# Optimization experiments

Hardware: AMD Instinct MI355X
Metric: run time of the kernel (lower is better)

Reference implementation:

```python
import jax, jax.numpy as jnp
import numpy as np

B, L, D, OUT, EXP = 4, 4096, 128, 55, 2
D2 = 2 * D

def _ln(x, g, b):
    m = jnp.mean(x, axis=-1, keepdims=True)
    v = jnp.mean((x - m) ** 2, axis=-1, keepdims=True)
    return (x - m) / jnp.sqrt(v + 1e-5) * g + b

def setup_inputs() -> dict:
    key = jax.random.key(0)
    ks = iter(jax.random.split(key, 32))
    w = lambda shape: jax.random.normal(next(ks), shape, jnp.float32) * 0.02
    inp = {
        'x1': jax.random.normal(next(ks), (B, L, D), jnp.float32),
        'x2': jax.random.normal(next(ks), (B, L, D), jnp.float32),
        'ln1_g': jnp.ones((D,)), 'ln1_b': jnp.zeros((D,)),
        'ln2_g': jnp.ones((D,)), 'ln2_b': jnp.zeros((D,)),
        'Wq': w((D, D)), 'bq': jnp.zeros((D,)),
        'Wv1': w((D, D)), 'bv1': jnp.zeros((D,)),
        'Wk': w((D, D)), 'bk': jnp.zeros((D,)),
        'Wv2': w((D, D)), 'bv2': jnp.zeros((D,)),
        'Wp1': w((D, D)), 'bp1': jnp.zeros((D,)),
        'Wp2': w((D, D)), 'bp2': jnp.zeros((D,)),
        'lnf_g': jnp.ones((D2,)), 'lnf_b': jnp.zeros((D2,)),
        'Wf1': w((D2, EXP * D2)), 'bf1': jnp.zeros((EXP * D2,)),
        'Wf2': w((EXP * D2, D2)), 'bf2': jnp.zeros((D2,)),
        'ln3_g': jnp.ones((D2,)), 'ln3_b': jnp.zeros((D2,)),
        'Wo': w((D2, OUT)), 'bo': jnp.zeros((OUT,)),
    }
    return inp

def reference(x1, x2, ln1_g, ln1_b, ln2_g, ln2_b, Wq, bq, Wv1, bv1, Wk, bk,
              Wv2, bv2, Wp1, bp1, Wp2, bp2, lnf_g, lnf_b, Wf1, bf1, Wf2, bf2,
              ln3_g, ln3_b, Wo, bo):
    res1, res2 = x1, x2
    x1n = _ln(x1, ln1_g, ln1_b)
    x2n = _ln(x2, ln2_g, ln2_b)
    q1 = x1n @ Wq + bq        # [B,L,D]
    v1 = x1n @ Wv1 + bv1
    k2 = x2n @ Wk + bk
    v2 = x2n @ Wv2 + bv2
    # faithful to torch: energy = einsum('bqd,bkd->bqk', keys2, queries1)
    energy = jnp.einsum('bqd,bkd->bqk', k2, q1)
    att = jax.nn.softmax(energy / jnp.sqrt(jnp.float32(D)), axis=-1)  # [B,L,L]
    out1 = jnp.einsum('bal,blv->bav', att, v1) @ Wp1 + bp1
    out2 = jnp.einsum('bal,blv->bav', att, v2) @ Wp2 + bp2
    y1 = out1 + res1
    y2 = out2 + res2
    x = jnp.concatenate([y1, y2], axis=-1)  # [B,L,2D]
    res = x
    h = _ln(x, lnf_g, lnf_b)
    h = jax.nn.gelu(h @ Wf1 + bf1, approximate=False) @ Wf2 + bf2
    x = _ln(h + res, ln3_g, ln3_b)
    return x @ Wo + bo  # [B,L,OUT]
```

## Files before the change

### kernel.cpp

```cpp
#include <hip/hip_runtime.h>
#include <hip/hip_fp16.h>

typedef _Float16 half8 __attribute__((ext_vector_type(8)));
typedef _Float16 half4 __attribute__((ext_vector_type(4)));
typedef float f32x4 __attribute__((ext_vector_type(4)));
typedef float f32x16 __attribute__((ext_vector_type(16)));
typedef int  i32x8 __attribute__((ext_vector_type(8)));
typedef long lng2 __attribute__((ext_vector_type(2)));

#define B_   4
#define L_   4096
#define D_   128
#define M_   (B_*L_)
#define D2_  256
#define H_   512
#define OUT_ 55

__device__ __forceinline__ f32x4 mfma16(half8 a, half8 b, f32x4 c) {
    return __builtin_amdgcn_mfma_f32_16x16x32_f16(a, b, c, 0, 0, 0);
}
__device__ __forceinline__ f32x16 mfma_mx32(i32x8 a, i32x8 b, f32x16 c) {
    return __builtin_amdgcn_mfma_scale_f32_32x32x64_f8f6f4(a, b, c, 0, 0, 0, 127, 0, 127);
}
__device__ __forceinline__ int pk4(float a, float b, float c, float d) {
    int t = __builtin_amdgcn_cvt_pk_fp8_f32(a, b, 0, false);
    return __builtin_amdgcn_cvt_pk_fp8_f32(c, d, t, true);
}
__device__ __forceinline__ float fexp2(float x) { return __builtin_amdgcn_exp2f(x); }

#define KSCL (0.08838834764831845f * 1.4426950408889634f)

#define WQ_OFF   0
#define WV1_OFF  16384
#define WK_OFF   32768
#define WV2_OFF  49152
#define WP1_OFF  65536
#define WP2_OFF  81920
#define WF1_OFF  98304
#define WF2_OFF  229376
#define WO_OFF   360448


__global__ void prep_kernel(const float* Wq, const float* Wv1, const float* Wk,
                            const float* Wv2, const float* Wp1, const float* Wp2,
                            const float* Wf1, const float* Wf2, const float* Wo,
                            _Float16* wsw, float* rowsum) {
    int id = blockIdx.y;
    int t  = blockIdx.x * 256 + threadIdx.x;
    if (id == 9) {
        if (t < 4096) ((f32x4*)rowsum)[t] = f32x4{0.f, 0.f, 0.f, 0.f};
        return;
    }
    const float* src = nullptr; int K = 0, N = 0, Npad = 0, off = 0;
    switch (id) {
        case 0: src = Wq;  K = 128; N = 128; Npad = 128; off = WQ_OFF;  break;
        case 1: src = Wv1; K = 128; N = 128; Npad = 128; off = WV1_OFF; break;
        case 2: src = Wk;  K = 128; N = 128; Npad = 128; off = WK_OFF;  break;
        case 3: src = Wv2; K = 128; N = 128; Npad = 128; off = WV2_OFF; break;
        case 4: src = Wp1; K = 128; N = 128; Npad = 128; off = WP1_OFF; break;
        case 5: src = Wp2; K = 128; N = 128; Npad = 128; off = WP2_OFF; break;
        case 6: src = Wf1; K = 256; N = 512; Npad = 512; off = WF1_OFF; break;
        case 7: src = Wf2; K = 512; N = 256; Npad = 256; off = WF2_OFF; break;
        case 8: src = Wo;  K = 256; N = 55;  Npad = 64;  off = WO_OFF;  break;
        default: return;
    }
    int total = K * Npad;
    if (t >= total) return;
    int k = t / Npad, n = t % Npad;
    float v = (n < N) ? src[k * N + n] : 0.f;
    int s = k >> 5, c = n >> 4, ln = n & 15;
    int q, j;
    if (id == 4 || id == 5) { q = (k >> 2) & 3; j = (k & 3) + (((k >> 4) & 1) << 2); }
    else                    { q = (k >> 3) & 3; j = k & 7; }
    int nc = Npad >> 4;
    wsw[off + ((size_t)((s * nc + c) * 64 + q * 16 + ln)) * 8 + j] = (_Float16)v;
}


__global__ __launch_bounds__(256) void proj_kernel(const float* x1, const float* x2,
        const _Float16* wsw,
        const float* ln1_g, const float* ln1_b, const float* ln2_g, const float* ln2_b,
        const float* bq, const float* bv1, const float* bk, const float* bv2,
        _Float16* q1, _Float16* k2, unsigned char* vsw8) {
    int g2 = blockIdx.y;
    const float* X  = g2 ? x2 : x1;
    const float* lg = g2 ? ln2_g : ln1_g;
    const float* lb = g2 ? ln2_b : ln1_b;
    int wave = threadIdx.x >> 6, lane = threadIdx.x & 63;
    int quad = lane >> 4, ln = lane & 15;
    int mbase = blockIdx.x * 64 + wave * 16;
    int lt = mbase >> 4;

    const float* xr = X + (size_t)(mbase + ln) * D_;
    float xv[4][8];
    float sum = 0.f, sq = 0.f;
    #pragma unroll
    for (int s = 0; s < 4; s++) {
        f32x4 v0 = *(const f32x4*)(xr + s * 32 + quad * 8);
        f32x4 v1 = *(const f32x4*)(xr + s * 32 + quad * 8 + 4);
        #pragma unroll
        for (int j = 0; j < 4; j++) {
            xv[s][j]     = v0[j];
            xv[s][j + 4] = v1[j];
            sum += v0[j] + v1[j];
            sq  += v0[j] * v0[j] + v1[j] * v1[j];
        }
    }
    sum += __shfl_xor(sum, 16); sum += __shfl_xor(sum, 32);
    sq  += __shfl_xor(sq, 16);  sq  += __shfl_xor(sq, 32);
    float mean = sum * (1.f / 128.f);
    float var  = sq * (1.f / 128.f) - mean * mean;
    float inv  = rsqrtf(var + 1e-5f);
    half8 a[4];
    #pragma unroll
    for (int s = 0; s < 4; s++) {
        f32x4 g0 = *(const f32x4*)(lg + s * 32 + quad * 8);
        f32x4 g1 = *(const f32x4*)(lg + s * 32 + quad * 8 + 4);
        f32x4 b0 = *(const f32x4*)(lb + s * 32 + quad * 8);
        f32x4 b1 = *(const f32x4*)(lb + s * 32 + quad * 8 + 4);
        #pragma unroll
        for (int j = 0; j < 4; j++) {
            a[s][j]     = (_Float16)((xv[s][j] - mean) * inv * g0[j] + b0[j]);
            a[s][j + 4] = (_Float16)((xv[s][j + 4] - mean) * inv * g1[j] + b1[j]);
        }
    }

    {
        const _Float16* Bw = wsw + (g2 ? WK_OFF : WQ_OFF);
        const float* bias = g2 ? bk : bq;
        float scl = g2 ? KSCL : 1.f;
        _Float16* out = g2 ? k2 : q1;
        f32x4 acc[8];
        #pragma unroll
        for (int c = 0; c < 8; c++) acc[c] = f32x4{0.f, 0.f, 0.f, 0.f};
        half8 Wc[4], Wn[4];
        #pragma unroll
        for (int s = 0; s < 4; s++)
            Wc[s] = *(const half8*)(Bw + ((size_t)((s * 8 + 0) * 64 + lane)) * 8);
        #pragma unroll
        for (int c = 0; c < 8; c++) {
            int cn = (c < 7) ? c + 1 : 7;
            #pragma unroll
            for (int s = 0; s < 4; s++)
                Wn[s] = *(const half8*)(Bw + ((size_t)((s * 8 + cn) * 64 + lane)) * 8);
            #pragma unroll
            for (int s = 0; s < 4; s++)
                acc[c] = mfma16(a[s], Wc[s], acc[c]);
            #pragma unroll
            for (int s = 0; s < 4; s++) Wc[s] = Wn[s];
        }
        #pragma unroll
        for (int c = 0; c < 8; c++) {
            int n = c * 16 + ln;
            float bv = bias[n];
            #pragma unroll
            for (int r = 0; r < 4; r++) {
                int s_o = c >> 1, q_o = ((c & 1) << 1) | (ln >> 3), j = ln & 7;
                out[((size_t)((lt * 4 + s_o) * 64 + q_o * 16 + (quad * 4 + r))) * 8 + j]
                    = (_Float16)((acc[c][r] + bv) * scl);
            }
        }
    }

    {
        const _Float16* Bw = wsw + (g2 ? WV2_OFF : WV1_OFF);
        const float* bias = g2 ? bv2 : bv1;
        int cbase = g2 ? 8 : 0;
        f32x4 acc[8];
        #pragma unroll
        for (int c = 0; c < 8; c++) acc[c] = f32x4{0.f, 0.f, 0.f, 0.f};
        half8 Wc[4], Wn[4];
        #pragma unroll
        for (int s = 0; s < 4; s++)
            Wc[s] = *(const half8*)(Bw + ((size_t)((s * 8 + 0) * 64 + lane)) * 8);
        #pragma unroll
        for (int c = 0; c < 8; c++) {
            int cn = (c < 7) ? c + 1 : 7;
            #pragma unroll
            for (int s = 0; s < 4; s++)
                Wn[s] = *(const half8*)(Bw + ((size_t)((s * 8 + cn) * 64 + lane)) * 8);
            #pragma unroll
            for (int s = 0; s < 4; s++)
                acc[c] = mfma16(a[s], Wc[s], acc[c]);
            #pragma unroll
            for (int s = 0; s < 4; s++) Wc[s] = Wn[s];
        }
        int b = mbase >> 12;
        int k64 = (mbase & (L_ - 1)) >> 6;
        int gg = quad >> 1, jh = quad & 1;
        unsigned char* Vb = vsw8 + (size_t)b * (1u << 20);
        #pragma unroll
        for (int c = 0; c < 8; c++) {
            int n = c * 16 + ln;
            float bv = bias[n];
            int pk = pk4(acc[c][0] + bv, acc[c][1] + bv, acc[c][2] + bv, acc[c][3] + bv);
            int v32 = (cbase + c) >> 1;
            int lane32 = ((c & 1) << 4) + ln + 32 * gg;
            *(int*)(Vb + ((size_t)((k64 * 8 + v32) * 64 + lane32)) * 32 + 16 * jh + 4 * wave) = pk;
        }
    }
}

__global__ __launch_bounds__(256) void score_kernel(
        const _Float16* __restrict__ q1sw, const _Float16* __restrict__ k2sw,
        unsigned char* __restrict__ pmat8, float* __restrict__ rowsum) {
    int w = threadIdx.x >> 6, lane = threadIdx.x & 63;
    int quad = lane >> 4, ln = lane & 15;
    int b = blockIdx.z;
    int id0 = blockIdx.y * 32 + blockIdx.x;
    int id  = ((id0 & 7) << 7) + (id0 >> 3);
    int bx = id & 31, by = id >> 5;
    int kL0 = by * 128 + (w & 1) * 64;
    int mL0 = bx * 128 + (w >> 1) * 64;
    int ltk = ((b << 12) + kL0) >> 4;
    int ltm = ((b << 12) + mL0) >> 4;

    f32x4 acc[4][4];
    #pragma unroll
    for (int i = 0; i < 4; i++)
        #pragma unroll
        for (int j = 0; j < 4; j++) acc[i][j] = f32x4{0.f, 0.f, 0.f, 0.f};

    #pragma unroll
    for (int s = 0; s < 4; s++) {
        half8 a[4], bq[4];
        #pragma unroll
        for (int i = 0; i < 4; i++)
            a[i] = *(const half8*)(q1sw + ((size_t)(((ltk + i) * 4 + s) * 64 + lane)) * 8);
        #pragma unroll
        for (int j = 0; j < 4; j++)
            bq[j] = *(const half8*)(k2sw + ((size_t)(((ltm + j) * 4 + s) * 64 + lane)) * 8);
        #pragma unroll
        for (int i = 0; i < 4; i++)
            #pragma unroll
            for (int j = 0; j < 4; j++)
                acc[i][j] = mfma16(a[i], bq[j], acc[i][j]);
    }

    unsigned char* Pb = pmat8 + (size_t)b * (16u << 20);
    int k64 = kL0 >> 6;
    int gg = quad >> 1, jh = quad & 1;
    #pragma unroll
    for (int j = 0; j < 4; j++) {
        int4 d;
        float csum = 0.f;
        #pragma unroll
        for (int i = 0; i < 4; i++) {
            float p0 = fexp2(acc[i][j][0]);
            float p1 = fexp2(acc[i][j][1]);
            float p2 = fexp2(acc[i][j][2]);
            float p3 = fexp2(acc[i][j][3]);
            csum += (p0 + p1) + (p2 + p3);
            ((int*)&d)[i] = pk4(p0, p1, p2, p3);
        }
        csum += __shfl_xor(csum, 16);
        csum += __shfl_xor(csum, 32);
        if (lane < 16)
            atomicAdd(&rowsum[(b << 12) + mL0 + j * 16 + ln], csum);
        int att32 = (mL0 >> 5) + (j >> 1);
        int a32 = ((j & 1) << 4) + ln;
        *(int4*)(Pb + ((size_t)((att32 * 64 + k64) * 64 + a32 + 32 * gg)) * 32 + 16 * jh) = d;
    }
}

__global__ __launch_bounds__(512) void pv_kernel(
        const unsigned char* __restrict__ pmat8, const unsigned char* __restrict__ vsw8,
        const float* __restrict__ rowsum,
        _Float16* __restrict__ att1, _Float16* __restrict__ att2) {
    __shared__ f32x4 part[4][2][4][64];
    int w = threadIdx.x >> 6, lane = threadIdx.x & 63;
    int wc = w & 3, kh = w >> 2;
    int id0 = blockIdx.x;
    int bid = ((id0 & 7) << 6) + (id0 >> 3);
    int rowG0 = bid * 32;
    int b = rowG0 >> 12;
    int att32 = (rowG0 & (L_ - 1)) >> 5;
    const unsigned char* Pb = pmat8 + (size_t)b * (16u << 20);
    const unsigned char* Vb = vsw8 + (size_t)b * (1u << 20);

    const unsigned char* Vbase = Vb + (size_t)(wc * 2) * 2048 + (size_t)lane * 32;
    const unsigned char* Pbase = Pb + (size_t)att32 * 131072 + (size_t)lane * 32;
    int sp0 = kh * 32;

    f32x16 acc0, acc1;
    #pragma unroll
    for (int i = 0; i < 16; i++) { acc0[i] = 0.f; acc1[i] = 0.f; }

    #define PVLOAD(dA, dB, dP, sp) do {                                       \
        dA = *(const i32x8*)(Vbase + (size_t)(sp) * 16384);                   \
        dB = *(const i32x8*)(Vbase + (size_t)(sp) * 16384 + 2048);            \
        dP = *(const i32x8*)(Pbase + (size_t)(sp) * 2048);                    \
    } while (0)

    i32x8 a0, b0, p0, a1, b1, p1, na, nb, np;
    PVLOAD(a0, b0, p0, sp0);
    PVLOAD(a1, b1, p1, sp0 + 1);
    for (int ii = 0; ii < 32; ii += 2) {
        int s2 = sp0 + ((ii + 2 < 32) ? ii + 2 : 30);
        int s3 = sp0 + ((ii + 3 < 32) ? ii + 3 : 31);
        PVLOAD(na, nb, np, s2);
        __builtin_amdgcn_s_setprio(1);
        acc0 = mfma_mx32(a0, p0, acc0);
        acc1 = mfma_mx32(b0, p0, acc1);
        __builtin_amdgcn_s_setprio(0);
        a0 = na; b0 = nb; p0 = np;
        PVLOAD(na, nb, np, s3);
        __builtin_amdgcn_s_setprio(1);
        acc0 = mfma_mx32(a1, p1, acc0);
        acc1 = mfma_mx32(b1, p1, acc1);
        __builtin_amdgcn_s_setprio(0);
        a1 = na; b1 = nb; p1 = np;
    }
    #undef PVLOAD

    if (kh == 1) {
        #pragma unroll
        for (int q = 0; q < 4; q++) {
            part[wc][0][q][lane] = f32x4{acc0[q * 4 + 0], acc0[q * 4 + 1],
                                         acc0[q * 4 + 2], acc0[q * 4 + 3]};
            part[wc][1][q][lane] = f32x4{acc1[q * 4 + 0], acc1[q * 4 + 1],
                                         acc1[q * 4 + 2], acc1[q * 4 + 3]};
        }
    }
    __syncthreads();
    if (kh == 0) {
        int aglob = rowG0 + (lane & 31);
        float inv = 1.f / rowsum[aglob];
        int g = lane >> 5;
        int lt = aglob >> 4, lnr = lane & 15;
        #pragma unroll
        for (int t = 0; t < 2; t++) {
            int v32 = wc * 2 + t;
            _Float16* att = (v32 >= 4) ? att2 : att1;
            int s = v32 & 3;
            #pragma unroll
            for (int q = 0; q < 4; q++) {
                f32x4 pp = part[wc][t][q][lane];
                half4 hv;
                #pragma unroll
                for (int rr = 0; rr < 4; rr++) {
                    float v = ((t == 0) ? acc0[q * 4 + rr] : acc1[q * 4 + rr]) + pp[rr];
                    hv[rr] = (_Float16)(v * inv);
                }
                *(half4*)(att + ((size_t)((lt * 4 + s) * 64 + q * 16 + lnr)) * 8 + 4 * g) = hv;
            }
        }
    }
}

__global__ __launch_bounds__(256) void attn_out_kernel(const _Float16* att1, const _Float16* att2,
        const _Float16* wsw, const float* bp1, const float* bp2,
        const float* x1, const float* x2, const float* lnf_g, const float* lnf_b,
        _Float16* res, _Float16* xn) {
    __shared__ float sst[2][16][2][2];
    int w = threadIdx.x >> 6, lane = threadIdx.x & 63;
    int quad = lane >> 4, ln = lane & 15;
    int rt = w & 1, st = w >> 1;
    int mbase = blockIdx.x * 32 + rt * 16;
    int lt = mbase >> 4;
    const _Float16* att = st ? att2 : att1;
    const _Float16* Wp = wsw + (st ? WP2_OFF : WP1_OFF);
    const float* bp = st ? bp2 : bp1;
    const float* xres = st ? x2 : x1;

    half8 a[4];
    #pragma unroll
    for (int s = 0; s < 4; s++)
        a[s] = *(const half8*)(att + ((size_t)((lt * 4 + s) * 64 + lane)) * 8);

    f32x4 y[8];
    #pragma unroll
    for (int c = 0; c < 8; c++) y[c] = f32x4{0,0,0,0};

    half8 Wc[4], Wn[4];
    #pragma unroll
    for (int s = 0; s < 4; s++)
        Wc[s] = *(const half8*)(Wp + ((size_t)((s * 8 + 0) * 64 + lane)) * 8);
    #pragma unroll
    for (int c = 0; c < 8; c++) {
        int cn = (c < 7) ? c + 1 : 7;
        #pragma unroll
        for (int s = 0; s < 4; s++)
            Wn[s] = *(const half8*)(Wp + ((size_t)((s * 8 + cn) * 64 + lane)) * 8);
        #pragma unroll
        for (int s = 0; s < 4; s++)
            y[c] = mfma16(a[s], Wc[s], y[c]);
        #pragma unroll
        for (int s = 0; s < 4; s++) Wc[s] = Wn[s];
    }

    float psum[4] = {0,0,0,0}, psq[4] = {0,0,0,0};
    #pragma unroll
    for (int c = 0; c < 8; c++) {
        int n = c * 16 + ln;
        float bv = bp[n];
        #pragma unroll
        for (int r = 0; r < 4; r++) {
            int m = mbase + quad * 4 + r;
            float v = y[c][r] + bv + xres[(size_t)m * D_ + n];
            y[c][r] = v; psum[r] += v; psq[r] += v * v;
        }
    }
    #pragma unroll
    for (int off = 1; off < 16; off <<= 1)
        #pragma unroll
        for (int r = 0; r < 4; r++) { psum[r] += __shfl_xor(psum[r], off); psq[r] += __shfl_xor(psq[r], off); }
    if (ln == 0)
        #pragma unroll
        for (int r = 0; r < 4; r++) {
            sst[rt][quad * 4 + r][st][0] = psum[r];
            sst[rt][quad * 4 + r][st][1] = psq[r];
        }
    __syncthreads();
    #pragma unroll
    for (int r = 0; r < 4; r++) {
        float su = sst[rt][quad * 4 + r][0][0] + sst[rt][quad * 4 + r][1][0];
        float sq = sst[rt][quad * 4 + r][0][1] + sst[rt][quad * 4 + r][1][1];
        float mean = su * (1.f / 256.f);
        float var = sq * (1.f / 256.f) - mean * mean;
        float inv = rsqrtf(var + 1e-5f);
        int m = mbase + quad * 4 + r;
        int lt_m = m >> 4;
        #pragma unroll
        for (int c = 0; c < 8; c++) {
            int colg = st * 128 + c * 16 + ln;
            res[(size_t)m * D2_ + colg] = (_Float16)y[c][r];
            float yn = (y[c][r] - mean) * inv * lnf_g[colg] + lnf_b[colg];
            int s_x = colg >> 5, q_x = (colg >> 3) & 3, j = colg & 7;
            xn[((size_t)((lt_m * 8 + s_x) * 64 + q_x * 16 + (m & 15))) * 8 + j] = (_Float16)yn;
        }
    }
}

__global__ __launch_bounds__(512) void ffn_kernel(const _Float16* xn, const _Float16* wsw,
        const float* bf1, const float* bf2, const _Float16* res,
        const float* g3, const float* b3, const float* bo, float* out) {
    __shared__ _Float16 hT[16384];
    __shared__ float sst[2][16][4][2];
    __shared__ _Float16 xt[8192];
    __shared__ f32x4 pc[2][3][4][64];
    int w = threadIdx.x >> 6, lane = threadIdx.x & 63;
    int quad = lane >> 4, ln = lane & 15;
    int rt = w & 1, nh = w >> 1;
    int mb = blockIdx.x * 32;
    int ltg = (mb + rt * 16) >> 4;

    {
        const _Float16* W = wsw + WF1_OFF;
        half8 a[8];
        #pragma unroll
        for (int s = 0; s < 8; s++)
            a[s] = *(const half8*)(xn + ((size_t)((ltg * 8 + s) * 64 + lane)) * 8);
        f32x4 acc[8];
        #pragma unroll
        for (int c = 0; c < 8; c++) acc[c] = f32x4{0,0,0,0};
        #pragma unroll
        for (int c = 0; c < 8; c++) {
            #pragma unroll
            for (int s = 0; s < 8; s++) {
                half8 Wf = *(const half8*)(W + ((size_t)((s * 32 + nh * 8 + c) * 64 + lane)) * 8);
                acc[c] = mfma16(a[s], Wf, acc[c]);
            }
        }
        #pragma unroll
        for (int c = 0; c < 8; c++) {
            int n = nh * 128 + c * 16 + ln;
            float bv = bf1[n];
            int s_h = n >> 5, q_h = (n >> 3) & 3, j = n & 7;
            #pragma unroll
            for (int r = 0; r < 4; r++) {
                float v = acc[c][r] + bv;
                float u = 0.7978845608f * (v + 0.044715f * v * v * v);
                float e = fexp2(-2.8853900818f * u);
                float ge = v * __builtin_amdgcn_rcpf(1.f + e);
                hT[((rt * 16 + s_h) * 64 + q_h * 16 + (quad * 4 + r)) * 8 + j] = (_Float16)ge;
            }
        }
    }
    __syncthreads();

    float y[4][4];
    {
        const _Float16* W = wsw + WF2_OFF;
        f32x4 acc[4];
        #pragma unroll
        for (int c = 0; c < 4; c++) acc[c] = f32x4{0,0,0,0};
        #pragma unroll
        for (int s = 0; s < 16; s++) {
            half8 a = *(const half8*)(hT + ((size_t)((rt * 16 + s) * 64 + lane)) * 8);
            #pragma unroll
            for (int c = 0; c < 4; c++) {
                half8 Wf = *(const half8*)(W + ((size_t)((s * 16 + nh * 4 + c) * 64 + lane)) * 8);
                acc[c] = mfma16(a, Wf, acc[c]);
            }
        }
        float psum[4] = {0,0,0,0}, psq[4] = {0,0,0,0};
        #pragma unroll
        for (int c = 0; c < 4; c++) {
            int n = nh * 64 + c * 16 + ln;
            float bv = bf2[n];
            #pragma unroll
            for (int r = 0; r < 4; r++) {
                int m = mb + rt * 16 + quad * 4 + r;
                float v = acc[c][r] + bv + (float)res[(size_t)m * D2_ + n];
                y[c][r] = v; psum[r] += v; psq[r] += v * v;
            }
        }
        #pragma unroll
        for (int off = 1; off < 16; off <<= 1)
            #pragma unroll
            for (int r = 0; r < 4; r++) { psum[r] += __shfl_xor(psum[r], off); psq[r] += __shfl_xor(psq[r], off); }
        if (ln == 0)
            #pragma unroll
            for (int r = 0; r < 4; r++) { sst[rt][quad * 4 + r][nh][0] = psum[r]; sst[rt][quad * 4 + r][nh][1] = psq[r]; }
    }
    __syncthreads();
    #pragma unroll
    for (int r = 0; r < 4; r++) {
        int row = quad * 4 + r;
        float su = sst[rt][row][0][0] + sst[rt][row][1][0] + sst[rt][row][2][0] + sst[rt][row][3][0];
        float sq = sst[rt][row][0][1] + sst[rt][row][1][1] + sst[rt][row][2][1] + sst[rt][row][3][1];
        float mean = su * (1.f / 256.f);
        float var = sq * (1.f / 256.f) - mean * mean;
        float invs = rsqrtf(var + 1e-5f);
        #pragma unroll
        for (int c = 0; c < 4; c++) {
            int n = nh * 64 + c * 16 + ln;
            float yn = (y[c][r] - mean) * invs * g3[n] + b3[n];
            int s_x = n >> 5, q_x = (n >> 3) & 3, j = n & 7;
            xt[((rt * 8 + s_x) * 64 + q_x * 16 + row) * 8 + j] = (_Float16)yn;
        }
    }
    __syncthreads();

    {
        int kh = nh;
        const _Float16* Wo = wsw + WO_OFF;
        f32x4 oacc[4];
        #pragma unroll
        for (int c = 0; c < 4; c++) oacc[c] = f32x4{0,0,0,0};
        #pragma unroll
        for (int ss = 0; ss < 2; ss++) {
            int s = kh * 2 + ss;
            half8 a = *(const half8*)(xt + ((size_t)((rt * 8 + s) * 64 + lane)) * 8);
            #pragma unroll
            for (int c = 0; c < 4; c++)
                oacc[c] = mfma16(a, *(const half8*)(Wo + ((size_t)((s * 4 + c) * 64 + lane)) * 8), oacc[c]);
        }
        if (kh > 0)
            #pragma unroll
            for (int c = 0; c < 4; c++) pc[rt][kh - 1][c][lane] = oacc[c];
        __syncthreads();
        if (kh == 0) {
            #pragma unroll
            for (int c = 0; c < 4; c++) {
                f32x4 p0 = pc[rt][0][c][lane];
                f32x4 p1 = pc[rt][1][c][lane];
                f32x4 p2 = pc[rt][2][c][lane];
                int n = c * 16 + ln;
                if (n < OUT_) {
                    float bv = bo[n];
                    #pragma unroll
                    for (int r = 0; r < 4; r++)
                        out[(size_t)(mb + rt * 16 + quad * 4 + r) * OUT_ + n]
                            = oacc[c][r] + p0[r] + p1[r] + p2[r] + bv;
                }
            }
        }
    }
}

extern "C" void kernel_launch(void* const* d_in, const int* in_sizes, int n_in,
                              void* d_out, int out_size, void* d_ws, size_t ws_size,
                              hipStream_t stream) {
    const float* x1    = (const float*)d_in[0];
    const float* x2    = (const float*)d_in[1];
    const float* ln1_g = (const float*)d_in[2];
    const float* ln1_b = (const float*)d_in[3];
    const float* ln2_g = (const float*)d_in[4];
    const float* ln2_b = (const float*)d_in[5];
    const float* Wq    = (const float*)d_in[6];
    const float* bq    = (const float*)d_in[7];
    const float* Wv1   = (const float*)d_in[8];
    const float* bv1   = (const float*)d_in[9];
    const float* Wk    = (const float*)d_in[10];
    const float* bk    = (const float*)d_in[11];
    const float* Wv2   = (const float*)d_in[12];
    const float* bv2   = (const float*)d_in[13];
    const float* Wp1   = (const float*)d_in[14];
    const float* bp1   = (const float*)d_in[15];
    const float* Wp2   = (const float*)d_in[16];
    const float* bp2   = (const float*)d_in[17];
    const float* lnf_g = (const float*)d_in[18];
    const float* lnf_b = (const float*)d_in[19];
    const float* Wf1   = (const float*)d_in[20];
    const float* bf1   = (const float*)d_in[21];
    const float* Wf2   = (const float*)d_in[22];
    const float* bf2   = (const float*)d_in[23];
    const float* ln3_g = (const float*)d_in[24];
    const float* ln3_b = (const float*)d_in[25];
    const float* Wo    = (const float*)d_in[26];
    const float* bo    = (const float*)d_in[27];
    float* out = (float*)d_out;

    char* ws = (char*)d_ws;
    const size_t MB = 1 << 20;
    _Float16* q1sw   = (_Float16*)(ws + 0 * MB);
    _Float16* k2sw   = (_Float16*)(ws + 4 * MB);
    unsigned char* vsw8 = (unsigned char*)(ws + 8 * MB);
    _Float16* att1   = (_Float16*)(ws + 12 * MB);
    _Float16* att2   = (_Float16*)(ws + 16 * MB);
    _Float16* wsw    = (_Float16*)(ws + 28 * MB);
    float*    rowsum = (float*)   (ws + 29 * MB);
    _Float16* res    = (_Float16*)(ws + 30 * MB);
    _Float16* xn     = (_Float16*)(ws + 46 * MB);
    unsigned char* pmat8 = (unsigned char*)(ws + 78 * MB);

    prep_kernel<<<dim3(512, 10), 256, 0, stream>>>(Wq, Wv1, Wk, Wv2, Wp1, Wp2, Wf1, Wf2, Wo,
                                                   wsw, rowsum);
    proj_kernel<<<dim3(M_ / 64, 2), 256, 0, stream>>>(x1, x2, wsw,
                                                      ln1_g, ln1_b, ln2_g, ln2_b,
                                                      bq, bv1, bk, bv2,
                                                      q1sw, k2sw, vsw8);
    score_kernel<<<dim3(32, 32, 4), 256, 0, stream>>>(q1sw, k2sw, pmat8, rowsum);
    pv_kernel<<<dim3(M_ / 32), 512, 0, stream>>>(pmat8, vsw8, rowsum, att1, att2);
    attn_out_kernel<<<dim3(M_ / 32), 256, 0, stream>>>(att1, att2, wsw, bp1, bp2,
                                                       x1, x2, lnf_g, lnf_b, res, xn);
    ffn_kernel<<<dim3(M_ / 32), 512, 0, stream>>>(xn, wsw, bf1, bf2, res,
                                                  ln3_g, ln3_b, bo, out);
}
```

Before: 228.4 us.

## Fuse attention output projection and residual LayerNorm into PV kernel epilogue

The attn_out kernel is merged into the PV kernel. The normalized attention rows now stay in shared memory instead of making a round trip through global att1/att2 buffers. The output projection is split across all 8 waves along K, with partial sums reduced through the reused shared buffer, then bias, residual, LayerNorm, res and xn stores follow. This removes one kernel launch and the global write and read of the attention output, at the cost of extra shared memory, more barriers, and a longer tail in the PV kernel that may lower occupancy.

```diff
diff --git a/kernel.cpp b/kernel.cpp
--- a/kernel.cpp
+++ b/kernel.cpp
@@ -6,7 +6,6 @@
 typedef float f32x4 __attribute__((ext_vector_type(4)));
 typedef float f32x16 __attribute__((ext_vector_type(16)));
 typedef int  i32x8 __attribute__((ext_vector_type(8)));
-typedef long lng2 __attribute__((ext_vector_type(2)));
 
 #define B_   4
 #define L_   4096
@@ -265,10 +264,15 @@
 
 __global__ __launch_bounds__(512) void pv_kernel(
         const unsigned char* __restrict__ pmat8, const unsigned char* __restrict__ vsw8,
-        const float* __restrict__ rowsum,
-        _Float16* __restrict__ att1, _Float16* __restrict__ att2) {
+        const float* __restrict__ rowsum, const _Float16* __restrict__ wsw,
+        const float* bp1, const float* bp2,
+        const float* x1, const float* x2, const float* lnf_g, const float* lnf_b,
+        _Float16* __restrict__ res, _Float16* __restrict__ xn) {
     __shared__ f32x4 part[4][2][4][64];
+    __shared__ _Float16 attT[2][4096];
+    __shared__ float sstA[2][16][2][2];
     int w = threadIdx.x >> 6, lane = threadIdx.x & 63;
+    int quad = lane >> 4, ln = lane & 15;
     int wc = w & 3, kh = w >> 2;
     int id0 = blockIdx.x;
     int bid = ((id0 & 7) << 6) + (id0 >> 3);
@@ -324,14 +328,14 @@
     }
     __syncthreads();
     if (kh == 0) {
-        int aglob = rowG0 + (lane & 31);
-        float inv = 1.f / rowsum[aglob];
+        int rowL = lane & 31;
+        float inv = 1.f / rowsum[rowG0 + rowL];
         int g = lane >> 5;
-        int lt = aglob >> 4, lnr = lane & 15;
+        int ltl = rowL >> 4, lnr = lane & 15;
         #pragma unroll
         for (int t = 0; t < 2; t++) {
             int v32 = wc * 2 + t;
-            _Float16* att = (v32 >= 4) ? att2 : att1;
+            int stw = (v32 >= 4);
             int s = v32 & 3;
             #pragma unroll
             for (int q = 0; q < 4; q++) {
@@ -342,92 +346,90 @@
                     float v = ((t == 0) ? acc0[q * 4 + rr] : acc1[q * 4 + rr]) + pp[rr];
                     hv[rr] = (_Float16)(v * inv);
                 }
-                *(half4*)(att + ((size_t)((lt * 4 + s) * 64 + q * 16 + lnr)) * 8 + 4 * g) = hv;
-            }
-        }
-    }
-}
-
-__global__ __launch_bounds__(256) void attn_out_kernel(const _Float16* att1, const _Float16* att2,
-        const _Float16* wsw, const float* bp1, const float* bp2,
-        const float* x1, const float* x2, const float* lnf_g, const float* lnf_b,
-        _Float16* res, _Float16* xn) {
-    __shared__ float sst[2][16][2][2];
-    int w = threadIdx.x >> 6, lane = threadIdx.x & 63;
-    int quad = lane >> 4, ln = lane & 15;
-    int rt = w & 1, st = w >> 1;
-    int mbase = blockIdx.x * 32 + rt * 16;
-    int lt = mbase >> 4;
-    const _Float16* att = st ? att2 : att1;
-    const _Float16* Wp = wsw + (st ? WP2_OFF : WP1_OFF);
-    const float* bp = st ? bp2 : bp1;
-    const float* xres = st ? x2 : x1;
-
-    half8 a[4];
-    #pragma unroll
-    for (int s = 0; s < 4; s++)
-        a[s] = *(const half8*)(att + ((size_t)((lt * 4 + s) * 64 + lane)) * 8);
-
-    f32x4 y[8];
-    #pragma unroll
-    for (int c = 0; c < 8; c++) y[c] = f32x4{0,0,0,0};
-
-    half8 Wc[4], Wn[4];
-    #pragma unroll
-    for (int s = 0; s < 4; s++)
-        Wc[s] = *(const half8*)(Wp + ((size_t)((s * 8 + 0) * 64 + lane)) * 8);
-    #pragma unroll
-    for (int c = 0; c < 8; c++) {
-        int cn = (c < 7) ? c + 1 : 7;
-        #pragma unroll
-        for (int s = 0; s < 4; s++)
-            Wn[s] = *(const half8*)(Wp + ((size_t)((s * 8 + cn) * 64 + lane)) * 8);
-        #pragma unroll
-        for (int s = 0; s < 4; s++)
-            y[c] = mfma16(a[s], Wc[s], y[c]);
-        #pragma unroll
-        for (int s = 0; s < 4; s++) Wc[s] = Wn[s];
-    }
-
-    float psum[4] = {0,0,0,0}, psq[4] = {0,0,0,0};
-    #pragma unroll
-    for (int c = 0; c < 8; c++) {
-        int n = c * 16 + ln;
-        float bv = bp[n];
-        #pragma unroll
-        for (int r = 0; r < 4; r++) {
-            int m = mbase + quad * 4 + r;
-            float v = y[c][r] + bv + xres[(size_t)m * D_ + n];
-            y[c][r] = v; psum[r] += v; psq[r] += v * v;
-        }
-    }
-    #pragma unroll
-    for (int off = 1; off < 16; off <<= 1)
-        #pragma unroll
-        for (int r = 0; r < 4; r++) { psum[r] += __shfl_xor(psum[r], off); psq[r] += __shfl_xor(psq[r], off); }
-    if (ln == 0)
-        #pragma unroll
-        for (int r = 0; r < 4; r++) {
-            sst[rt][quad * 4 + r][st][0] = psum[r];
-            sst[rt][quad * 4 + r][st][1] = psq[r];
-        }
+                *(half4*)(&attT[stw][((ltl * 4 + s) * 64 + q * 16 + lnr) * 8 + 4 * g]) = hv;
+            }
+        }
+    }
     __syncthreads();
-    #pragma unroll
-    for (int r = 0; r < 4; r++) {
-        float su = sst[rt][quad * 4 + r][0][0] + sst[rt][quad * 4 + r][1][0];
-        float sq = sst[rt][quad * 4 + r][0][1] + sst[rt][quad * 4 + r][1][1];
-        float mean = su * (1.f / 256.f);
-        float var = sq * (1.f / 256.f) - mean * mean;
-        float inv = rsqrtf(var + 1e-5f);
-        int m = mbase + quad * 4 + r;
-        int lt_m = m >> 4;
+
+    {
+        int rt = w & 1, st = (w >> 1) & 1, kh2 = w >> 2;
+        const _Float16* Wp = wsw + (st ? WP2_OFF : WP1_OFF);
+        const float* bp = st ? bp2 : bp1;
+        const float* xres = st ? x2 : x1;
+
+        half8 a2[2];
+        #pragma unroll
+        for (int ss = 0; ss < 2; ss++)
+            a2[ss] = *(const half8*)(&attT[st][((rt * 4 + kh2 * 2 + ss) * 64 + lane) * 8]);
+
+        f32x4 y[8];
+        #pragma unroll
+        for (int c = 0; c < 8; c++) y[c] = f32x4{0,0,0,0};
         #pragma unroll
         for (int c = 0; c < 8; c++) {
-            int colg = st * 128 + c * 16 + ln;
-            res[(size_t)m * D2_ + colg] = (_Float16)y[c][r];
-            float yn = (y[c][r] - mean) * inv * lnf_g[colg] + lnf_b[colg];
-            int s_x = colg >> 5, q_x = (colg >> 3) & 3, j = colg & 7;
-            xn[((size_t)((lt_m * 8 + s_x) * 64 + q_x * 16 + (m & 15))) * 8 + j] = (_Float16)yn;
+            #pragma unroll
+            for (int ss = 0; ss < 2; ss++) {
+                half8 Wf = *(const half8*)(Wp + ((size_t)(((kh2 * 2 + ss) * 8 + c) * 64 + lane)) * 8);
+                y[c] = mfma16(a2[ss], Wf, y[c]);
+            }
+        }
+        f32x4 (*partC)[2][8][64] = (f32x4(*)[2][8][64])&part[0][0][0][0];
+        if (kh2 == 1) {
+            #pragma unroll
+            for (int c = 0; c < 8; c++) partC[rt][st][c][lane] = y[c];
+        }
+        __syncthreads();
+        float yy[8][4];
+        if (kh2 == 0) {
+            float psum[4] = {0,0,0,0}, psq[4] = {0,0,0,0};
+            #pragma unroll
+            for (int c = 0; c < 8; c++) {
+                f32x4 pp = partC[rt][st][c][lane];
+                int n = c * 16 + ln;
+                float bv = bp[n];
+                #pragma unroll
+                for (int r = 0; r < 4; r++) {
+                    int m = rowG0 + rt * 16 + quad * 4 + r;
+                    float v = y[c][r] + pp[r] + bv + xres[(size_t)m * D_ + n];
+                    yy[c][r] = v; psum[r] += v; psq[r] += v * v;
+                }
+            }
+            #pragma unroll
+            for (int off = 1; off < 16; off <<= 1)
+                #pragma unroll
+                for (int r = 0; r < 4; r++) {
+                    psum[r] += __shfl_xor(psum[r], off);
+                    psq[r]  += __shfl_xor(psq[r], off);
+                }
+            if (ln == 0)
+                #pragma unroll
+                for (int r = 0; r < 4; r++) {
+                    sstA[rt][quad * 4 + r][st][0] = psum[r];
+                    sstA[rt][quad * 4 + r][st][1] = psq[r];
+                }
+        }
+        __syncthreads();
+        if (kh2 == 0) {
+            #pragma unroll
+            for (int r = 0; r < 4; r++) {
+                int row = quad * 4 + r;
+                float su = sstA[rt][row][0][0] + sstA[rt][row][1][0];
+                float sq = sstA[rt][row][0][1] + sstA[rt][row][1][1];
+                float mean = su * (1.f / 256.f);
+                float var = sq * (1.f / 256.f) - mean * mean;
+                float invs = rsqrtf(var + 1e-5f);
+                int m = rowG0 + rt * 16 + row;
+                int lt_m = m >> 4;
+                #pragma unroll
+                for (int c = 0; c < 8; c++) {
+                    int colg = st * 128 + c * 16 + ln;
+                    res[(size_t)m * D2_ + colg] = (_Float16)yy[c][r];
+                    float yn = (yy[c][r] - mean) * invs * lnf_g[colg] + lnf_b[colg];
+                    int s_x = colg >> 5, q_x = (colg >> 3) & 3, j = colg & 7;
+                    xn[((size_t)((lt_m * 8 + s_x) * 64 + q_x * 16 + (m & 15))) * 8 + j] = (_Float16)yn;
+                }
+            }
         }
     }
 }
@@ -608,8 +610,6 @@
     _Float16* q1sw   = (_Float16*)(ws + 0 * MB);
     _Float16* k2sw   = (_Float16*)(ws + 4 * MB);
     unsigned char* vsw8 = (unsigned char*)(ws + 8 * MB);
-    _Float16* att1   = (_Float16*)(ws + 12 * MB);
-    _Float16* att2   = (_Float16*)(ws + 16 * MB);
     _Float16* wsw    = (_Float16*)(ws + 28 * MB);
     float*    rowsum = (float*)   (ws + 29 * MB);
     _Float16* res    = (_Float16*)(ws + 30 * MB);
@@ -623,9 +623,9 @@
                                                       bq, bv1, bk, bv2,
                                                       q1sw, k2sw, vsw8);
     score_kernel<<<dim3(32, 32, 4), 256, 0, stream>>>(q1sw, k2sw, pmat8, rowsum);
-    pv_kernel<<<dim3(M_ / 32), 512, 0, stream>>>(pmat8, vsw8, rowsum, att1, att2);
-    attn_out_kernel<<<dim3(M_ / 32), 256, 0, stream>>>(att1, att2, wsw, bp1, bp2,
-                                                       x1, x2, lnf_g, lnf_b, res, xn);
+    pv_kernel<<<dim3(M_ / 32), 512, 0, stream>>>(pmat8, vsw8, rowsum, wsw,
+                                                 bp1, bp2, x1, x2, lnf_g, lnf_b,
+                                                 res, xn);
     ffn_kernel<<<dim3(M_ / 32), 512, 0, stream>>>(xn, wsw, bf1, bf2, res,
                                                   ln3_g, ln3_b, bo, out);
 }
```

New measurement: 228.1 us. About the same (-0.2%).
